# Performance work log

Hardware: AMD Instinct MI355X
Metric: run time of the kernel (lower is better)

The kernel has to match this reference:

```python
import jax, jax.numpy as jnp
import numpy as np

B, S, D, H, DFF = 4, 2048, 512, 8, 2048
HD = D // H  # head dim = 64
LN_EPS = 1e-5


def setup_inputs() -> dict:
    key = jax.random.key(0)
    ks = jax.random.split(key, 12)
    sc = 0.02
    return {
        "x": jax.random.normal(ks[0], (B, S, D), jnp.float32),
        "Wq": jax.random.normal(ks[1], (D, D), jnp.float32) * sc,
        "bq": jnp.zeros((D,), jnp.float32),
        "Wk": jax.random.normal(ks[2], (D, D), jnp.float32) * sc,
        "bk": jnp.zeros((D,), jnp.float32),
        "Wv": jax.random.normal(ks[3], (D, D), jnp.float32) * sc,
        "bv": jnp.zeros((D,), jnp.float32),
        "W1": jax.random.normal(ks[4], (D, DFF), jnp.float32) * sc,
        "b1": jnp.zeros((DFF,), jnp.float32),
        "W2": jax.random.normal(ks[5], (DFF, D), jnp.float32) * sc,
        "b2": jnp.zeros((D,), jnp.float32),
        "gamma": jnp.ones((D,), jnp.float32),
        "beta": jnp.zeros((D,), jnp.float32),
    }


def reference(x, Wq, bq, Wk, bk, Wv, bv, W1, b1, W2, b2, gamma, beta):
    # Multi-head self-attention (explicit bmm -> softmax -> bmm chain)
    q = (x @ Wq + bq).reshape(B, S, H, HD)
    k = (x @ Wk + bk).reshape(B, S, H, HD)
    v = (x @ Wv + bv).reshape(B, S, H, HD)
    scores = jnp.einsum("bqhd,bkhd->bhqk", q, k) / jnp.sqrt(jnp.float32(HD))
    atn = jax.nn.softmax(scores, axis=-1)          # [B,H,S,S]
    attn_out = jnp.einsum("bhqk,bkhd->bqhd", atn, v).reshape(B, S, D)
    # FFN with residual + LayerNorm (residual around FFN only, as in source)
    h = jax.nn.relu(attn_out @ W1 + b1)
    y = h @ W2 + b2 + attn_out
    mu = jnp.mean(y, axis=-1, keepdims=True)
    var = jnp.var(y, axis=-1, keepdims=True)
    out = (y - mu) * jax.lax.rsqrt(var + LN_EPS) * gamma + beta
    return (out, atn)
```

## Files before the change

kernel.cpp:

```cpp
#include <hip/hip_runtime.h>
#include <hip/hip_bf16.h>

#define TPB 256
typedef long long ll;


using short8  = __attribute__((ext_vector_type(8))) short;
using short4v = __attribute__((ext_vector_type(4))) short;
using floatx4 = __attribute__((ext_vector_type(4))) float;

__device__ __forceinline__ unsigned short f2bu(float f) {
    union { float f; unsigned int u; } v; v.f = f;
    unsigned int u = v.u;
    return (unsigned short)((u + 0x7fffu + ((u >> 16) & 1u)) >> 16);
}

__device__ __forceinline__ float bu2f(unsigned short us) {
    union { unsigned int u; float f; } v; v.u = ((unsigned int)us) << 16;
    return v.f;
}

__device__ __forceinline__ unsigned int cvtpk(float lo, float hi) {
    unsigned int r;
    asm volatile("v_cvt_pk_bf16_f32 %0, %1, %2" : "=v"(r) : "v"(lo), "v"(hi));
    return r;
}

__device__ __forceinline__ floatx4 mfma16(short4v a, short4v b, floatx4 c) {
#if __has_builtin(__builtin_amdgcn_mfma_f32_16x16x16bf16_1k)
    return __builtin_amdgcn_mfma_f32_16x16x16bf16_1k(a, b, c, 0, 0, 0);
#else
    floatx4 d;
    asm volatile("v_mfma_f32_16x16x16_bf16 %0, %1, %2, %3"
                 : "=v"(d) : "v"(a), "v"(b), "v"(c));
    return d;
#endif
}

__device__ __forceinline__ void gload16(const unsigned short* g, unsigned short* l) {
    __builtin_amdgcn_global_load_lds(
        (const __attribute__((address_space(1))) void*)g,
        (__attribute__((address_space(3))) void*)l, 16, 0, 0);
}

template<int BM, int BN, int EPI>
__device__ __forceinline__ void gemm_body(
    const unsigned short* __restrict__ Ap, const unsigned short* __restrict__ BTp,
    const float* __restrict__ bias, void* __restrict__ Cp,
    const unsigned short* __restrict__ Rb,
    int K, ll lda, ll ldb, ll ldc, int bx, int by,
    unsigned short* Asm, unsigned short* Bsm)
{
    constexpr int BK = 64;
    const int tid  = threadIdx.x;
    const int lane = tid & 63;
    const int wave = tid >> 6;
    const int wm = wave >> 1, wn = wave & 1;
    constexpr int WM = BM / 2, WN = BN / 2, FM = WM / 16, FN = WN / 16;

    const ll brow = (ll)bx * BM;
    const ll bcol = (ll)by * BN;
    const int srow = lane >> 3;
    const int ssw  = (((lane & 7) ^ srow)) << 3;
    const int kswz = (lane & 7) << 3;

    floatx4 acc[FM][FN] = {};

    for (int k0 = 0; k0 < K; k0 += BK) {
        #pragma unroll
        for (int ii = 0; ii < BM / 32; ++ii) {
            int i = wave + ii * 4;
            gload16(Ap + (brow + i * 8 + srow) * lda + k0 + ssw, Asm + i * 512);
        }
        #pragma unroll
        for (int ii = 0; ii < BN / 32; ++ii) {
            int i = wave + ii * 4;
            gload16(BTp + (bcol + i * 8 + srow) * ldb + k0 + ssw, Bsm + i * 512);
        }
        __syncthreads();

        #pragma unroll
        for (int kk = 0; kk < BK; kk += 32) {
            short8 af[FM], bfr[FN];
            const int kidx = (kk + ((lane >> 4) << 3)) ^ kswz;
            const int ar = wm * WM + (lane & 15);
            const int bc = wn * WN + (lane & 15);
            #pragma unroll
            for (int m = 0; m < FM; m++)
                af[m] = *(const short8*)&Asm[(ar + m * 16) * BK + kidx];
            #pragma unroll
            for (int n = 0; n < FN; n++)
                bfr[n] = *(const short8*)&Bsm[(bc + n * 16) * BK + kidx];
            #pragma unroll
            for (int m = 0; m < FM; m++)
                #pragma unroll
                for (int n = 0; n < FN; n++)
                    acc[m][n] = __builtin_amdgcn_mfma_f32_16x16x32_bf16(af[m], bfr[n], acc[m][n], 0, 0, 0);
        }
        __syncthreads();
    }

    const ll crow0 = brow + wm * WM + ((lane >> 4) << 2);
    const ll ccol0 = bcol + wn * WN + (lane & 15);
    #pragma unroll
    for (int m = 0; m < FM; m++) {
        #pragma unroll
        for (int j = 0; j < 4; j++) {
            ll row = crow0 + m * 16 + j;
            #pragma unroll
            for (int np = 0; np < FN; np += 2) {
                ll col0 = ccol0 + np * 16;
                ll col1 = col0 + 16;
                float v0 = acc[m][np][j]     + bias[col0];
                float v1 = acc[m][np + 1][j] + bias[col1];
                if constexpr (EPI == 3) {
                    v0 = v0 > 0.f ? v0 : 0.f;
                    v1 = v1 > 0.f ? v1 : 0.f;
                } else if constexpr (EPI == 6) {
                    v0 += bu2f(Rb[row * ldc + col0]);
                    v1 += bu2f(Rb[row * ldc + col1]);
                } else if constexpr (EPI == 7) {
                    if (col0 < 512) v0 *= 0.125f;
                    if (col1 < 512) v1 *= 0.125f;
                }
                unsigned int r = cvtpk(v0, v1);
                ((unsigned short*)Cp)[row * ldc + col0] = (unsigned short)r;
                ((unsigned short*)Cp)[row * ldc + col1] = (unsigned short)(r >> 16);
            }
        }
    }
}

template<int BM, int BN, int EPI>
__global__ __launch_bounds__(TPB) void gemm_k(
    const unsigned short* __restrict__ Ap, const unsigned short* __restrict__ BTp,
    const float* __restrict__ bias, void* __restrict__ Cp,
    const unsigned short* __restrict__ Rb,
    int K, ll lda, ll ldb, ll ldc)
{
    __shared__ unsigned short sh[BM * 64 + BN * 64];
    int nwg = gridDim.x * gridDim.y;
    int sid = blockIdx.y * gridDim.x + blockIdx.x;
    int cpx = nwg >> 3;
    int w = (sid & 7) * cpx + (sid >> 3);
    int bx = w % gridDim.x, by = w / gridDim.x;
    gemm_body<BM, BN, EPI>(Ap, BTp, bias, Cp, Rb, K, lda, ldb, ldc, bx, by,
                           sh, sh + BM * 64);
}

__device__ __forceinline__ void atnwrite_body(
    const unsigned short* __restrict__ qkv, const float* __restrict__ ilbuf,
    float* __restrict__ atn, int BH0, int n, unsigned short* sh)
{
    unsigned short* Qsm = sh;
    unsigned short* Ksm = sh + 8192;
    float* Pst = (float*)sh;

    const int tid = threadIdx.x, lane = tid & 63, wave = tid >> 6;
    const int c0 = lane & 15, g = lane >> 4;
    const int bh = BH0 + (n & 7) * 2 + ((n >> 3) & 1);
    const int qt = n >> 4;
    const int b = bh >> 3, h = bh & 7;

    const ll qbase  = ((ll)(b * 2048 + qt * 128)) * 1536 + h * 64;
    const ll kbase0 = ((ll)(b * 2048)) * 1536 + 512 + h * 64;
    const int srow = lane >> 3;
    const int ssw  = (((lane & 7) ^ srow)) << 3;
    const int kswz = (lane & 7) << 3;

    #pragma unroll
    for (int ii = 0; ii < 4; ++ii) {
        int i = wave + ii * 4;
        gload16(qkv + qbase + (ll)(i * 8 + srow) * 1536 + ssw, Qsm + i * 512);
    }
    __syncthreads();
    short8 qf[2][2];
    #pragma unroll
    for (int nq = 0; nq < 2; nq++)
        #pragma unroll
        for (int kk = 0; kk < 2; kk++)
            qf[nq][kk] = *(const short8*)&Qsm[(wave * 32 + nq * 16 + c0) * 64 + ((kk * 32 + g * 8) ^ kswz)];

    float il2[2];
    #pragma unroll
    for (int nq = 0; nq < 2; nq++)
        il2[nq] = ilbuf[(ll)bh * 2048 + qt * 128 + wave * 32 + nq * 16 + c0];

    float* myP = Pst + wave * 1024;

    for (int kb = 0; kb < 16; ++kb) {
        const ll koff = kbase0 + (ll)kb * 128 * 1536;
        #pragma unroll
        for (int ii = 0; ii < 4; ++ii) {
            int i = wave + ii * 4;
            gload16(qkv + koff + (ll)(i * 8 + srow) * 1536 + ssw, Ksm + i * 512);
        }
        __syncthreads();

        floatx4 sacc[8][2] = {};
        #pragma unroll
        for (int kk = 0; kk < 2; kk++)
            #pragma unroll
            for (int mk = 0; mk < 8; mk++) {
                short8 kf = *(const short8*)&Ksm[(mk * 16 + c0) * 64 + ((kk * 32 + g * 8) ^ kswz)];
                #pragma unroll
                for (int nq = 0; nq < 2; nq++)
                    sacc[mk][nq] = __builtin_amdgcn_mfma_f32_16x16x32_bf16(kf, qf[nq][kk], sacc[mk][nq], 0, 0, 0);
            }

        #pragma unroll
        for (int mk = 0; mk < 8; mk++)
            #pragma unroll
            for (int nq = 0; nq < 2; nq++)
                #pragma unroll
                for (int r = 0; r < 4; r++)
                    sacc[mk][nq][r] = __expf(sacc[mk][nq][r]) * il2[nq];

        #pragma unroll
        for (int nq = 0; nq < 2; nq++) {
            #pragma unroll
            for (int hf = 0; hf < 2; hf++) {
                if ((c0 >> 3) == hf) {
                    int rho = c0 & 7;
                    #pragma unroll
                    for (int mk = 0; mk < 8; mk++) {
                        int k4 = mk * 4 + g;
                        ((floatx4*)myP)[rho * 32 + (k4 ^ rho)] = sacc[mk][nq];
                    }
                }
                const ll grow = (ll)bh * 2048 + qt * 128 + wave * 32 + nq * 16 + hf * 8;
                #pragma unroll
                for (int t = 0; t < 4; t++) {
                    int rr = t * 2 + (lane >> 5);
                    int k4r = lane & 31;
                    floatx4 v = ((const floatx4*)myP)[rr * 32 + (k4r ^ rr)];
                    __builtin_nontemporal_store(
                        v, (floatx4*)(atn + (grow + rr) * 2048 + kb * 128 + k4r * 4));
                }
            }
        }
        __syncthreads();
    }
}

__global__ __launch_bounds__(TPB) void attn1_k(
    const unsigned short* __restrict__ qkv, const unsigned short* __restrict__ vt,
    unsigned short* __restrict__ attnb, float* __restrict__ ilbuf)
{
    __shared__ unsigned short sh[32768];

    const int tid = threadIdx.x, lane = tid & 63, wave = tid >> 6;
    const int c0 = lane & 15, g = lane >> 4;
    const int srow = lane >> 3;
    const int ssw  = (((lane & 7) ^ srow)) << 3;
    const int kswz = (lane & 7) << 3;

    const int raw = blockIdx.x + blockIdx.y * 16;
    const int n   = raw >> 3;
    const int bh  = (raw & 7) * 4 + (n >> 4);
    const int qt  = n & 15;
    const int b = bh >> 3, h = bh & 7;

    const ll qbase  = ((ll)(b * 2048 + qt * 128)) * 1536 + h * 64;
    const ll kbase0 = ((ll)(b * 2048)) * 1536 + 512 + h * 64;
    const unsigned short* vbase = vt + (ll)bh * 64 * 2048;

    #pragma unroll
    for (int ii = 0; ii < 4; ++ii) {
        int i = wave + ii * 4;
        gload16(qkv + qbase + (ll)(i * 8 + srow) * 1536 + ssw, sh + i * 512);
    }
    __syncthreads();
    short8 qf[2][2];
    #pragma unroll
    for (int nq = 0; nq < 2; nq++)
        #pragma unroll
        for (int kk = 0; kk < 2; kk++)
            qf[nq][kk] = *(const short8*)&sh[(wave * 32 + nq * 16 + c0) * 64 + ((kk * 32 + g * 8) ^ kswz)];
    __syncthreads();

    floatx4 oaccT[4][2] = {};
    float l_run[2] = {0.f, 0.f};

#define STAGE_KV(kbx, bb) do {                                                   \
    const ll koff_ = kbase0 + (ll)(kbx) * 128 * 1536;                            \
    unsigned short* Kd_ = sh + ((bb) << 13);                                     \
    unsigned short* Vd_ = sh + 16384 + ((bb) << 13);                             \
    _Pragma("unroll")                                                            \
    for (int ii = 0; ii < 4; ++ii) { int i = wave + ii * 4;                      \
        gload16(qkv + koff_ + (ll)(i * 8 + srow) * 1536 + ssw, Kd_ + i * 512); } \
    _Pragma("unroll")                                                            \
    for (int ii = 0; ii < 4; ++ii) { int i = wave + ii * 4; int s = i * 8 + srow;\
        int vrow = s >> 1; int vslot = ((s & 1) << 3) | (lane & 7);              \
        gload16(vbase + (ll)vrow * 2048 + (kbx) * 128 + ((vslot ^ (vrow & 7)) << 3), \
                Vd_ + i * 512); }                                                \
} while (0)

    STAGE_KV(0, 0);
    for (int kb = 0; kb < 16; ++kb) {
        const int cur = kb & 1;
        if (kb < 15) {
            STAGE_KV(kb + 1, cur ^ 1);
            asm volatile("s_waitcnt vmcnt(8)" ::: "memory");
        } else {
            asm volatile("s_waitcnt vmcnt(0)" ::: "memory");
        }
        __builtin_amdgcn_sched_barrier(0);
        __builtin_amdgcn_s_barrier();
        __builtin_amdgcn_sched_barrier(0);

        unsigned short* Kc = sh + (cur << 13);
        unsigned short* Vc = sh + 16384 + (cur << 13);

        floatx4 sacc[8][2] = {};
        #pragma unroll
        for (int kk = 0; kk < 2; kk++)
            #pragma unroll
            for (int mk = 0; mk < 8; mk++) {
                short8 kf = *(const short8*)&Kc[(mk * 16 + c0) * 64 + ((kk * 32 + g * 8) ^ kswz)];
                #pragma unroll
                for (int nq = 0; nq < 2; nq++)
                    sacc[mk][nq] = __builtin_amdgcn_mfma_f32_16x16x32_bf16(kf, qf[nq][kk], sacc[mk][nq], 0, 0, 0);
            }

        #pragma unroll
        for (int nq = 0; nq < 2; nq++) {
            float rs = 0.f;
            #pragma unroll
            for (int mk = 0; mk < 8; mk++)
                #pragma unroll
                for (int r = 0; r < 4; r++) {
                    float p = __expf(sacc[mk][nq][r]);
                    sacc[mk][nq][r] = p;
                    rs += p;
                }
            rs += __shfl_xor(rs, 16);
            rs += __shfl_xor(rs, 32);
            l_run[nq] += rs;
        }

        #pragma unroll
        for (int mk = 0; mk < 8; mk++) {
            short4v pb[2];
            #pragma unroll
            for (int nq = 0; nq < 2; nq++) {
                union { unsigned int u[2]; short4v s; } pu;
                pu.u[0] = cvtpk(sacc[mk][nq][0], sacc[mk][nq][1]);
                pu.u[1] = cvtpk(sacc[mk][nq][2], sacc[mk][nq][3]);
                pb[nq] = pu.s;
            }
            #pragma unroll
            for (int mk2 = 0; mk2 < 4; mk2++) {
                short4v vf = *(const short4v*)&Vc[(mk2 * 16 + c0) * 128 + ((mk * 16 + g * 4) ^ kswz)];
                #pragma unroll
                for (int nq = 0; nq < 2; nq++)
                    oaccT[mk2][nq] = mfma16(vf, pb[nq], oaccT[mk2][nq]);
            }
        }
        __builtin_amdgcn_sched_barrier(0);
        __builtin_amdgcn_s_barrier();
        __builtin_amdgcn_sched_barrier(0);
    }
#undef STAGE_KV

    const float il[2] = { 1.0f / l_run[0], 1.0f / l_run[1] };

    #pragma unroll
    for (int nq = 0; nq < 2; nq++) {
        int qrow = qt * 128 + wave * 32 + nq * 16 + c0;
        ll row = (ll)b * 2048 + qrow;
        #pragma unroll
        for (int mk2 = 0; mk2 < 4; mk2++) {
            int col = h * 64 + mk2 * 16 + g * 4;
            unsigned int r0 = cvtpk(oaccT[mk2][nq][0] * il[nq], oaccT[mk2][nq][1] * il[nq]);
            unsigned int r1 = cvtpk(oaccT[mk2][nq][2] * il[nq], oaccT[mk2][nq][3] * il[nq]);
            int2 tb = { (int)r0, (int)r1 };
            *(int2*)&attnb[row * 512 + col] = tb;
        }
        if (g == 0) ilbuf[(ll)bh * 2048 + qrow] = il[nq];
    }
}

template<int BH0, int GX, int GY, int BM, int BN, int EPI>
__global__ __launch_bounds__(TPB) void fused_k(
    const unsigned short* __restrict__ qkv, const float* __restrict__ ilbuf,
    float* __restrict__ atn,
    const unsigned short* __restrict__ Ap, const unsigned short* __restrict__ BTp,
    const float* __restrict__ bias, void* __restrict__ Cp,
    const unsigned short* __restrict__ Rb,
    int K, ll lda, ll ldb, ll ldc)
{
    __shared__ unsigned short sh[16384];
    const int bid = blockIdx.x;
    if (bid < 256) {
        atnwrite_body(qkv, ilbuf, atn, BH0, bid, sh);
    } else {
        int sid = bid - 256;
        constexpr int NWG = GX * GY;
        int w = (sid & 7) * (NWG >> 3) + (sid >> 3);
        int bx = w % GX, by = w / GX;
        gemm_body<BM, BN, EPI>(Ap, BTp, bias, Cp, Rb, K, lda, ldb, ldc, bx, by,
                               sh, sh + BM * 64);
    }
}

__global__ __launch_bounds__(TPB) void ln_k(const unsigned short* __restrict__ y,
                                            const float* __restrict__ gamma,
                                            const float* __restrict__ beta,
                                            float* __restrict__ out)
{
    const int lane = threadIdx.x & 63;
    const ll row = (ll)blockIdx.x * 4 + (threadIdx.x >> 6);
    short8 v = *(const short8*)(y + row * 512 + lane * 8);
    float f[8];
    float s = 0.f, q = 0.f;
    #pragma unroll
    for (int j = 0; j < 8; j++) {
        f[j] = bu2f((unsigned short)v[j]);
        s += f[j]; q += f[j] * f[j];
    }
    #pragma unroll
    for (int off = 32; off; off >>= 1) { s += __shfl_xor(s, off); q += __shfl_xor(q, off); }
    const float mu  = s * (1.0f / 512.0f);
    const float var = q * (1.0f / 512.0f) - mu * mu;
    const float rs  = rsqrtf(var + 1e-5f);

    float4 g0 = *(const float4*)(gamma + lane * 8);
    float4 g1 = *(const float4*)(gamma + lane * 8 + 4);
    float4 e0 = *(const float4*)(beta  + lane * 8);
    float4 e1 = *(const float4*)(beta  + lane * 8 + 4);
    floatx4 o0, o1;
    o0[0] = (f[0] - mu) * rs * g0.x + e0.x;  o0[1] = (f[1] - mu) * rs * g0.y + e0.y;
    o0[2] = (f[2] - mu) * rs * g0.z + e0.z;  o0[3] = (f[3] - mu) * rs * g0.w + e0.w;
    o1[0] = (f[4] - mu) * rs * g1.x + e1.x;  o1[1] = (f[5] - mu) * rs * g1.y + e1.y;
    o1[2] = (f[6] - mu) * rs * g1.z + e1.z;  o1[3] = (f[7] - mu) * rs * g1.w + e1.w;
    __builtin_nontemporal_store(o0, (floatx4*)(out + row * 512 + lane * 8));
    __builtin_nontemporal_store(o1, (floatx4*)(out + row * 512 + lane * 8 + 4));
}

__global__ __launch_bounds__(TPB) void prep_k(
    const float* __restrict__ Wq, const float* __restrict__ Wk,
    const float* __restrict__ Wv, const float* __restrict__ W1,
    const float* __restrict__ W2,
    const float* __restrict__ bq, const float* __restrict__ bk,
    const float* __restrict__ bv, const float* __restrict__ x,
    unsigned short* __restrict__ wtqkv, unsigned short* __restrict__ wt1,
    unsigned short* __restrict__ wt2, float* __restrict__ bqkv,
    unsigned short* __restrict__ xb)
{
    __shared__ float t[32 * 33];
    const int bid = blockIdx.x;
    const float* W; unsigned short* WT; int K, N, tile;
    if (bid < 256)       { W = Wq; WT = wtqkv;             K = 512;  N = 512;  tile = bid; }
    else if (bid < 512)  { W = Wk; WT = wtqkv + 512 * 512; K = 512;  N = 512;  tile = bid - 256; }
    else if (bid < 768)  { W = Wv; WT = wtqkv + 1024 * 512;K = 512;  N = 512;  tile = bid - 512; }
    else if (bid < 1792) { W = W1; WT = wt1;               K = 512;  N = 2048; tile = bid - 768; }
    else if (bid < 2816) { W = W2; WT = wt2;               K = 2048; N = 512;  tile = bid - 1792; }
    else if (bid < 2822) {
        int i = (bid - 2816) * TPB + threadIdx.x;
        if (i < 512)       bqkv[i] = bq[i];
        else if (i < 1024) bqkv[i] = bk[i - 512];
        else if (i < 1536) bqkv[i] = bv[i - 1024];
        return;
    } else {
        ll i = ((ll)(bid - 2822) * TPB + threadIdx.x) * 4;
        float4 v = *(const float4*)(x + i);
        unsigned int r0 = cvtpk(v.x, v.y), r1 = cvtpk(v.z, v.w);
        int2 tt = { (int)r0, (int)r1 };
        *(int2*)(xb + i) = tt;
        return;
    }
    const int nx = N >> 5;
    const int n0 = (tile % nx) * 32, k0 = (tile / nx) * 32;
    const int tx = threadIdx.x & 31, ty = threadIdx.x >> 5;
    #pragma unroll
    for (int i = ty; i < 32; i += 8) t[i * 33 + tx] = W[(ll)(k0 + i) * N + n0 + tx];
    __syncthreads();
    #pragma unroll
    for (int i = ty; i < 32; i += 8) WT[(ll)(n0 + i) * K + k0 + tx] = f2bu(t[tx * 33 + i]);
}

__global__ __launch_bounds__(TPB) void transv_k(const unsigned short* __restrict__ qkv,
                                                unsigned short* __restrict__ vt)
{
    const int z = blockIdx.y;  const int b = z >> 3, h = z & 7;
    const int s0 = blockIdx.x * 64;
    __shared__ unsigned short t[64][72];
    const unsigned short* src = qkv + ((ll)(b * 2048 + s0)) * 1536 + 1024 + h * 64;
    for (int c = threadIdx.x; c < 512; c += TPB) {
        int r = c >> 3, c8 = (c & 7) << 3;
        *(int4*)&t[r][c8] = *(const int4*)(src + (ll)r * 1536 + c8);
    }
    __syncthreads();
    unsigned short* dst = vt + (ll)z * 64 * 2048 + s0;
    for (int c = threadIdx.x; c < 512; c += TPB) {
        int hd = c >> 3, s8 = (c & 7) << 3;
        unsigned short tmp[8];
        #pragma unroll
        for (int j = 0; j < 8; j++) tmp[j] = t[s8 + j][hd];
        *(int4*)(dst + (ll)hd * 2048 + s8) = *(const int4*)tmp;
    }
}

extern "C" void kernel_launch(void* const* d_in, const int* in_sizes, int n_in,
                              void* d_out, int out_size, void* d_ws, size_t ws_size,
                              hipStream_t stream)
{
    (void)in_sizes; (void)n_in; (void)out_size; (void)ws_size;
    const float* x     = (const float*)d_in[0];
    const float* Wq    = (const float*)d_in[1];
    const float* bq    = (const float*)d_in[2];
    const float* Wk    = (const float*)d_in[3];
    const float* bk    = (const float*)d_in[4];
    const float* Wv    = (const float*)d_in[5];
    const float* bv    = (const float*)d_in[6];
    const float* W1    = (const float*)d_in[7];
    const float* b1    = (const float*)d_in[8];
    const float* W2    = (const float*)d_in[9];
    const float* b2    = (const float*)d_in[10];
    const float* gamma = (const float*)d_in[11];
    const float* beta  = (const float*)d_in[12];

    char* ws = (char*)d_ws;
    size_t off = 0;
    auto alloc = [&](size_t bytes) -> char* {
        char* p = ws + off; off += (bytes + 255) & ~(size_t)255; return p;
    };
    unsigned short* xb    = (unsigned short*)alloc(8192ll * 512 * 2);
    unsigned short* wtqkv = (unsigned short*)alloc(1536ll * 512 * 2);
    unsigned short* wt1   = (unsigned short*)alloc(2048ll * 512 * 2);
    unsigned short* wt2   = (unsigned short*)alloc(512ll * 2048 * 2);
    float*          bqkv  = (float*)alloc(1536 * 4);
    unsigned short* qkv   = (unsigned short*)alloc(8192ll * 1536 * 2);
    unsigned short* vt    = (unsigned short*)alloc(32ll * 64 * 2048 * 2);
    unsigned short* attnb = (unsigned short*)alloc(8192ll * 512 * 2);
    unsigned short* hmid  = (unsigned short*)alloc(8192ll * 2048 * 2);
    unsigned short* ybuf  = (unsigned short*)alloc(8192ll * 512 * 2);
    float*          ilbuf = (float*)alloc(32ll * 2048 * 4);

    float* outp = (float*)d_out;
    float* atn  = outp + 4194304;

    prep_k<<<2822 + 4096, TPB, 0, stream>>>(Wq, Wk, Wv, W1, W2, bq, bk, bv, x,
                                            wtqkv, wt1, wt2, bqkv, xb);

    gemm_k<128, 128, 7><<<dim3(64, 12, 1), TPB, 0, stream>>>(
        xb, wtqkv, bqkv, qkv, nullptr, 512, 512, 512, 1536);

    transv_k<<<dim3(32, 32), TPB, 0, stream>>>(qkv, vt);

    attn1_k<<<dim3(16, 32), TPB, 0, stream>>>(qkv, vt, attnb, ilbuf);

    fused_k<0, 64, 16, 128, 128, 3><<<256 + 1024, TPB, 0, stream>>>(
        qkv, ilbuf, atn,
        attnb, wt1, b1, hmid, nullptr, 512, 512, 512, 2048);

    fused_k<16, 128, 4, 64, 128, 6><<<256 + 512, TPB, 0, stream>>>(
        qkv, ilbuf, atn,
        hmid, wt2, b2, ybuf, attnb, 2048, 2048, 2048, 512);

    ln_k<<<2048, TPB, 0, stream>>>(ybuf, gamma, beta, outp);
}
```

Measured before the change: 275.1 us.

## Split attention into two launches and overlap atn writes with second half

The single flash-attention launch becomes two. The first computes heads 0-15. The second runs the remaining heads together with the attention-probability write-out for heads 0-7, so the write-heavy blocks overlap the compute-bound attention blocks. The GEMM-fused kernels now each carry 12 head-groups of atn writes instead of 16. The intent is better load balance across CUs between memory-bound atn writing and compute. The cost is an extra kernel launch and a larger LDS footprint for the write blocks in the fused attention kernel.

```diff
diff --git a/kernel.cpp b/kernel.cpp
--- a/kernel.cpp
+++ b/kernel.cpp
@@ -150,7 +150,7 @@
 
 __device__ __forceinline__ void atnwrite_body(
     const unsigned short* __restrict__ qkv, const float* __restrict__ ilbuf,
-    float* __restrict__ atn, int BH0, int n, unsigned short* sh)
+    float* __restrict__ atn, int bh, int qt, unsigned short* sh)
 {
     unsigned short* Qsm = sh;
     unsigned short* Ksm = sh + 8192;
@@ -158,8 +158,6 @@
 
     const int tid = threadIdx.x, lane = tid & 63, wave = tid >> 6;
     const int c0 = lane & 15, g = lane >> 4;
-    const int bh = BH0 + (n & 7) * 2 + ((n >> 3) & 1);
-    const int qt = n >> 4;
     const int b = bh >> 3, h = bh & 7;
 
     const ll qbase  = ((ll)(b * 2048 + qt * 128)) * 1536 + h * 64;
@@ -243,22 +241,16 @@
     }
 }
 
-__global__ __launch_bounds__(TPB) void attn1_k(
+__device__ __forceinline__ void attn1_body(
     const unsigned short* __restrict__ qkv, const unsigned short* __restrict__ vt,
-    unsigned short* __restrict__ attnb, float* __restrict__ ilbuf)
-{
-    __shared__ unsigned short sh[32768];
-
+    unsigned short* __restrict__ attnb, float* __restrict__ ilbuf,
+    int bh, int qt, unsigned short* sh)
+{
     const int tid = threadIdx.x, lane = tid & 63, wave = tid >> 6;
     const int c0 = lane & 15, g = lane >> 4;
     const int srow = lane >> 3;
     const int ssw  = (((lane & 7) ^ srow)) << 3;
     const int kswz = (lane & 7) << 3;
-
-    const int raw = blockIdx.x + blockIdx.y * 16;
-    const int n   = raw >> 3;
-    const int bh  = (raw & 7) * 4 + (n >> 4);
-    const int qt  = n & 15;
     const int b = bh >> 3, h = bh & 7;
 
     const ll qbase  = ((ll)(b * 2048 + qt * 128)) * 1536 + h * 64;
@@ -381,8 +373,36 @@
     }
 }
 
-template<int BH0, int GX, int GY, int BM, int BN, int EPI>
-__global__ __launch_bounds__(TPB) void fused_k(
+__global__ __launch_bounds__(TPB) void attn1a_k(
+    const unsigned short* __restrict__ qkv, const unsigned short* __restrict__ vt,
+    unsigned short* __restrict__ attnb, float* __restrict__ ilbuf)
+{
+    __shared__ unsigned short sh[32768];
+    const int n = blockIdx.x;
+    const int bh = (n & 7) * 2 + ((n >> 3) & 1);
+    const int qt = n >> 4;
+    attn1_body(qkv, vt, attnb, ilbuf, bh, qt, sh);
+}
+
+__global__ __launch_bounds__(TPB) void fused1_k(
+    const unsigned short* __restrict__ qkv, const unsigned short* __restrict__ vt,
+    unsigned short* __restrict__ attnb, float* __restrict__ ilbuf,
+    float* __restrict__ atn)
+{
+    __shared__ unsigned short sh[32768];
+    const int bid = blockIdx.x;
+    if (bid < 128) {
+        atnwrite_body(qkv, ilbuf, atn, bid & 7, bid >> 3, sh);
+    } else {
+        const int m = bid - 128;
+        const int bh = 16 + (m & 7) * 2 + ((m >> 3) & 1);
+        const int qt = m >> 4;
+        attn1_body(qkv, vt, attnb, ilbuf, bh, qt, sh);
+    }
+}
+
+template<int WRBH0, int WRCNT, int GX, int GY, int BM, int BN, int EPI>
+__global__ __launch_bounds__(TPB) void fusedg_k(
     const unsigned short* __restrict__ qkv, const float* __restrict__ ilbuf,
     float* __restrict__ atn,
     const unsigned short* __restrict__ Ap, const unsigned short* __restrict__ BTp,
@@ -392,10 +412,11 @@
 {
     __shared__ unsigned short sh[16384];
     const int bid = blockIdx.x;
-    if (bid < 256) {
-        atnwrite_body(qkv, ilbuf, atn, BH0, bid, sh);
+    constexpr int WRN = WRCNT * 16;
+    if (bid < WRN) {
+        atnwrite_body(qkv, ilbuf, atn, WRBH0 + bid % WRCNT, bid / WRCNT, sh);
     } else {
-        int sid = bid - 256;
+        int sid = bid - WRN;
         constexpr int NWG = GX * GY;
         int w = (sid & 7) * (NWG >> 3) + (sid >> 3);
         int bx = w % GX, by = w / GX;
@@ -549,13 +570,15 @@
 
     transv_k<<<dim3(32, 32), TPB, 0, stream>>>(qkv, vt);
 
-    attn1_k<<<dim3(16, 32), TPB, 0, stream>>>(qkv, vt, attnb, ilbuf);
-
-    fused_k<0, 64, 16, 128, 128, 3><<<256 + 1024, TPB, 0, stream>>>(
+    attn1a_k<<<256, TPB, 0, stream>>>(qkv, vt, attnb, ilbuf);
+
+    fused1_k<<<384, TPB, 0, stream>>>(qkv, vt, attnb, ilbuf, atn);
+
+    fusedg_k<8, 12, 64, 16, 128, 128, 3><<<192 + 1024, TPB, 0, stream>>>(
         qkv, ilbuf, atn,
         attnb, wt1, b1, hmid, nullptr, 512, 512, 512, 2048);
 
-    fused_k<16, 128, 4, 64, 128, 6><<<256 + 512, TPB, 0, stream>>>(
+    fusedg_k<20, 12, 128, 4, 64, 128, 6><<<192 + 512, TPB, 0, stream>>>(
         qkv, ilbuf, atn,
         hmid, wt2, b2, ybuf, attnb, 2048, 2048, 2048, 512);
 
```

Measured after the change: 273.8 us. About the same (-0.5%).
